# Performance work log

Measured on AMD Instinct MI355X. Metric: run time of the kernel, lower is better.

Reference implementation:

```python
import jax, jax.numpy as jnp
import numpy as np


def setup_inputs() -> dict:
    key = jax.random.key(0)
    k1, k2, k3, k4 = jax.random.split(key, 4)
    B, L, V, F, D = 32, 4096, 10, 1024, 64
    indices = jax.random.randint(k1, (B, L), 0, V, dtype=jnp.int64)
    fp_table = jax.random.normal(k2, (V, F), dtype=jnp.float32)
    W = jax.random.normal(k3, (D, F), dtype=jnp.float32) * 0.03
    b = jax.random.normal(k4, (D,), dtype=jnp.float32) * 0.01
    return {"indices": indices, "fp_table": fp_table, "W": W, "b": b}


def reference(indices, fp_table, W, b):
    # Per-character fingerprint lookup: [B, L, F]
    emb = fp_table[indices]
    # Linear 1024 -> dim: [B, L, D]
    proj = jnp.einsum('blf,df->bld', emb, W) + b
    # Original: per-sequence [L, D] -> transpose -> [D, L]; vstack over batch -> [B*D, L];
    # reshape(-1, B*D, L) -> [1, B*D, L]
    B, L, D = proj.shape
    out = jnp.transpose(proj, (0, 2, 1)).reshape(B * D, L)
    return out.reshape(1, B * D, L)
```

## Files before the change

kernel.cpp:

```cpp
#include <hip/hip_runtime.h>

#define B_SIZE 32
#define L_SIZE 4096
#define V_SIZE 10
#define F_SIZE 1024
#define D_SIZE 64

__global__ __launch_bounds__(64) void fp_proj_kernel(
    const float* __restrict__ fp_table,
    const float* __restrict__ W,
    const float* __restrict__ bias,
    float* __restrict__ Pt) {
  const int o = blockIdx.x;
  const int v = o / D_SIZE;
  const int d = o % D_SIZE;
  const int lane = threadIdx.x;

  const float4* ft4 = (const float4*)(fp_table + v * F_SIZE);
  const float4* w4  = (const float4*)(W + d * F_SIZE);

  float sum = 0.f;
  for (int i = lane; i < F_SIZE / 4; i += 64) {
    float4 a = ft4[i];
    float4 b = w4[i];
    sum += a.x * b.x + a.y * b.y + a.z * b.z + a.w * b.w;
  }
  #pragma unroll
  for (int off = 32; off > 0; off >>= 1)
    sum += __shfl_down(sum, off, 64);

  if (lane == 0) Pt[d * V_SIZE + v] = sum + bias[d];
}

__global__ __launch_bounds__(256) void gather_kernel(
    const int* __restrict__ idx,
    const float* __restrict__ Pt,
    float* __restrict__ out) {
  __shared__ float Pl[D_SIZE * V_SIZE];
  for (int i = threadIdx.x; i < D_SIZE * V_SIZE; i += 256) Pl[i] = Pt[i];
  __syncthreads();

  const int g  = blockIdx.x * 256 + threadIdx.x;
  const int r  = g >> 10;
  const int c4 = g & 1023;
  const int b  = r >> 6;
  const int d  = r & 63;

  const int4 vi = ((const int4*)idx)[b * (L_SIZE / 4) + c4];

  const float* Pd = Pl + d * V_SIZE;
  float4 o;
  o.x = Pd[vi.x];
  o.y = Pd[vi.y];
  o.z = Pd[vi.z];
  o.w = Pd[vi.w];

  ((float4*)out)[g] = o;
}

extern "C" void kernel_launch(void* const* d_in, const int* in_sizes, int n_in,
                              void* d_out, int out_size, void* d_ws, size_t ws_size,
                              hipStream_t stream) {
  const int*   idx      = (const int*)d_in[0];
  const float* fp_table = (const float*)d_in[1];
  const float* W        = (const float*)d_in[2];
  const float* bias     = (const float*)d_in[3];
  float* out = (float*)d_out;
  float* Pt  = (float*)d_ws;

  fp_proj_kernel<<<V_SIZE * D_SIZE, 64, 0, stream>>>(fp_table, W, bias, Pt);

  const int total4 = B_SIZE * D_SIZE * (L_SIZE / 4);
  gather_kernel<<<total4 / 256, 256, 0, stream>>>(idx, Pt, out);
}
```

Baseline: 75.56 us.

## Fuse projection table computation into gather kernel with nontemporal stores

Merges the two kernels into one: each block (one output row b,d) recomputes the 10 projected values for its d by dot-producting W row d with all fingerprint rows, reduces them across four waves, then gathers 4096 outputs for that row. This removes a kernel launch and the global round-trip through the workspace. Output writes become nontemporal stores. In exchange the projection is recomputed redundantly 32 times per d, adding about 44KB of cached reads per block.

```diff
diff --git a/kernel.cpp b/kernel.cpp
--- a/kernel.cpp
+++ b/kernel.cpp
@@ -6,56 +6,59 @@
 #define F_SIZE 1024
 #define D_SIZE 64
 
-__global__ __launch_bounds__(64) void fp_proj_kernel(
+typedef float nt_float4 __attribute__((ext_vector_type(4)));
+
+__global__ __launch_bounds__(256) void fused_fp_embed_kernel(
+    const int* __restrict__ idx,
     const float* __restrict__ fp_table,
     const float* __restrict__ W,
     const float* __restrict__ bias,
-    float* __restrict__ Pt) {
-  const int o = blockIdx.x;
-  const int v = o / D_SIZE;
-  const int d = o % D_SIZE;
-  const int lane = threadIdx.x;
+    float* __restrict__ out) {
+  const int r   = blockIdx.x;
+  const int d   = r & 63;
+  const int b   = r >> 6;
+  const int tid = threadIdx.x;
+  const int lane = tid & 63;
+  const int wave = tid >> 6;
 
-  const float4* ft4 = (const float4*)(fp_table + v * F_SIZE);
-  const float4* w4  = (const float4*)(W + d * F_SIZE);
-
-  float sum = 0.f;
-  for (int i = lane; i < F_SIZE / 4; i += 64) {
-    float4 a = ft4[i];
-    float4 b = w4[i];
-    sum += a.x * b.x + a.y * b.y + a.z * b.z + a.w * b.w;
+  const float4 w4 = ((const float4*)(W + d * F_SIZE))[tid];
+  float s[V_SIZE];
+  #pragma unroll
+  for (int v = 0; v < V_SIZE; ++v) {
+    const float4 a = ((const float4*)(fp_table + v * F_SIZE))[tid];
+    s[v] = a.x * w4.x + a.y * w4.y + a.z * w4.z + a.w * w4.w;
   }
   #pragma unroll
-  for (int off = 32; off > 0; off >>= 1)
-    sum += __shfl_down(sum, off, 64);
-
-  if (lane == 0) Pt[d * V_SIZE + v] = sum + bias[d];
-}
-
-__global__ __launch_bounds__(256) void gather_kernel(
-    const int* __restrict__ idx,
-    const float* __restrict__ Pt,
-    float* __restrict__ out) {
-  __shared__ float Pl[D_SIZE * V_SIZE];
-  for (int i = threadIdx.x; i < D_SIZE * V_SIZE; i += 256) Pl[i] = Pt[i];
+  for (int v = 0; v < V_SIZE; ++v) {
+    #pragma unroll
+    for (int off = 32; off > 0; off >>= 1)
+      s[v] += __shfl_down(s[v], off, 64);
+  }
+  __shared__ float red[4][V_SIZE];
+  __shared__ float Pl[16];
+  if (lane == 0) {
+    #pragma unroll
+    for (int v = 0; v < V_SIZE; ++v) red[wave][v] = s[v];
+  }
+  __syncthreads();
+  if (tid < V_SIZE) {
+    Pl[tid] = red[0][tid] + red[1][tid] + red[2][tid] + red[3][tid] + bias[d];
+  }
   __syncthreads();
 
-  const int g  = blockIdx.x * 256 + threadIdx.x;
-  const int r  = g >> 10;
-  const int c4 = g & 1023;
-  const int b  = r >> 6;
-  const int d  = r & 63;
-
-  const int4 vi = ((const int4*)idx)[b * (L_SIZE / 4) + c4];
-
-  const float* Pd = Pl + d * V_SIZE;
-  float4 o;
-  o.x = Pd[vi.x];
-  o.y = Pd[vi.y];
-  o.z = Pd[vi.z];
-  o.w = Pd[vi.w];
-
-  ((float4*)out)[g] = o;
+  const int4* idxr = (const int4*)(idx + b * L_SIZE);
+  nt_float4* outr = (nt_float4*)(out + (size_t)r * L_SIZE);
+  #pragma unroll
+  for (int j = 0; j < 4; ++j) {
+    const int c4 = tid + 256 * j;
+    const int4 vi = idxr[c4];
+    nt_float4 o;
+    o.x = Pl[vi.x];
+    o.y = Pl[vi.y];
+    o.z = Pl[vi.z];
+    o.w = Pl[vi.w];
+    __builtin_nontemporal_store(o, outr + c4);
+  }
 }
 
 extern "C" void kernel_launch(void* const* d_in, const int* in_sizes, int n_in,
@@ -66,10 +69,7 @@
   const float* W        = (const float*)d_in[2];
   const float* bias     = (const float*)d_in[3];
   float* out = (float*)d_out;
-  float* Pt  = (float*)d_ws;
 
-  fp_proj_kernel<<<V_SIZE * D_SIZE, 64, 0, stream>>>(fp_table, W, bias, Pt);
-
-  const int total4 = B_SIZE * D_SIZE * (L_SIZE / 4);
-  gather_kernel<<<total4 / 256, 256, 0, stream>>>(idx, Pt, out);
+  fused_fp_embed_kernel<<<B_SIZE * D_SIZE, 256, 0, stream>>>(
+      idx, fp_table, W, bias, out);
 }
```

After: 75.66 us. Within noise of the previous version (+0.1%).
